# Kernel optimization log

Hardware: AMD Instinct MI355X
Metric: run time of the kernel (lower is better)

## Reference

```python
import jax, jax.numpy as jnp
import numpy as np

B, T, N, CIN, H, K, HOR = 64, 12, 800, 2, 64, 3, 12
TCOV_IN, TCOV_H, MNUM, MDIM = 60, 2, 4, 8
KAPPA = 0.05
IN0 = CIN + TCOV_H  # layer-0 input dim: data channels + time-covariate embedding


def setup_inputs() -> dict:
    key = jax.random.key(0)
    ks = jax.random.split(key, 24)
    def nrm(k, shape, s=0.1):
        return jax.random.normal(k, shape, jnp.float32) * s
    inp = {}
    inp["x_seq"] = jax.random.normal(ks[0], (B, T, N, CIN), jnp.float32)
    inp["t_x"] = jax.random.normal(ks[1], (B, T, TCOV_IN), jnp.float32)
    inp["t_y"] = jax.random.normal(ks[2], (B, HOR, TCOV_IN), jnp.float32)
    # adaptive graph as in init_adp_graph: softmax(relu(v1 @ v2), axis=1)
    inp["G"] = jax.nn.softmax(jax.nn.relu(nrm(ks[3], (N, 20), 1.0) @ nrm(ks[4], (20, N), 1.0)), axis=1)
    i = 5
    for pre in ("enc", "dec"):
        for l, hin in enumerate((IN0, H)):
            inp[f"{pre}_Wg{l}"] = nrm(ks[i], ((hin + H) * K, 2 * H)); i += 1
            inp[f"{pre}_bg{l}"] = jnp.zeros((2 * H,), jnp.float32)
            inp[f"{pre}_Wc{l}"] = nrm(ks[i], ((hin + H) * K, H)); i += 1
            inp[f"{pre}_bc{l}"] = jnp.zeros((H,), jnp.float32)
    inp["mlp_W1"] = nrm(ks[i], (TCOV_IN, 10)); i += 1
    inp["mlp_b1"] = jnp.zeros((10,), jnp.float32)
    inp["mlp_W2"] = nrm(ks[i], (10, TCOV_H * N)); i += 1
    inp["mlp_b2"] = jnp.zeros((TCOV_H * N,), jnp.float32)
    inp["memory"] = nrm(ks[i], (MNUM, MDIM), 1.0); i += 1
    inp["Wa"] = nrm(ks[i], (N * H, MDIM), 0.01); i += 1
    inp["fc"] = nrm(ks[i], (MDIM, MDIM * N), 0.1); i += 1
    inp["proj_W"] = nrm(ks[i], (H + MDIM, CIN)); i += 1
    inp["proj_b"] = jnp.zeros((CIN,), jnp.float32)
    return inp


def _cheby(G):
    # Chebyshev basis T_0..T_{K-1}: T_0=I, T_1=G, T_k = 2 G T_{k-1} - T_{k-2}
    Gs = [jnp.eye(N, dtype=G.dtype), G]
    for _ in range(2, K):
        Gs.append(2.0 * (G @ Gs[-1]) - Gs[-2])
    return jnp.stack(Gs[:K])  # (K, N, N)


def _gconv(x, Gs, W, b):
    # mixhop: h_k = kappa*x + (1-kappa) * einsum('bnp,nm->bmp', x, T_k); concat over k, then project
    agg = KAPPA * x[None] + (1.0 - KAPPA) * jnp.einsum('bnp,knm->kbmp', x, Gs)  # (K,B,N,P)
    Bq, Nq, P = x.shape
    h = jnp.transpose(agg, (1, 2, 0, 3)).reshape(Bq, Nq, K * P)  # matches torch.cat order
    return h @ W + b


def _cell(x, h, Gs, Wg, bg, Wc, bc):
    # GCRU cell: graph-conv GRU
    ur = _gconv(jnp.concatenate([x, h], -1), Gs, Wg, bg)
    u, r = jnp.split(ur, 2, axis=-1)
    u = jax.nn.sigmoid(u)
    r = jax.nn.sigmoid(r)
    c = jnp.tanh(_gconv(jnp.concatenate([x, r * h], -1), Gs, Wc, bc))
    return (1.0 - u) * h + u * c


def _mlp(t, W1, b1, W2, b2):
    # nn.Sequential(Linear, Linear) -- no activation in between
    return (t @ W1 + b1) @ W2 + b2


def reference(x_seq, t_x, t_y, G, enc_Wg0, enc_bg0, enc_Wc0, enc_bc0, enc_Wg1, enc_bg1, enc_Wc1, enc_bc1, dec_Wg0, dec_bg0, dec_Wc0, dec_bc0, dec_Wg1, dec_bg1, dec_Wc1, dec_bc1, mlp_W1, mlp_b1, mlp_W2, mlp_b2, memory, Wa, fc, proj_W, proj_b):
    Gs = _cheby(G)
    # time covariates for encoder input
    tx_emb = _mlp(t_x, mlp_W1, mlp_b1, mlp_W2, mlp_b2).reshape(B, T, N, TCOV_H)
    x = jnp.concatenate([x_seq, tx_emb], -1)  # (B,T,N,IN0)
    # encoder: scan over time per layer
    seq = jnp.swapaxes(x, 0, 1)  # (T,B,N,.)
    enc_params = [(enc_Wg0, enc_bg0, enc_Wc0, enc_bc0), (enc_Wg1, enc_bg1, enc_Wc1, enc_bc1)]
    h_last = []
    for (Wg, bg, Wc, bc) in enc_params:
        def step(h, xt, Wg=Wg, bg=bg, Wc=Wc, bc=bc):
            hn = _cell(xt, h, Gs, Wg, bg, Wc, bc)
            return hn, hn
        h0 = jnp.zeros((B, N, H), x.dtype)
        hT, seq = jax.lax.scan(step, h0, seq)
        h_last.append(hT)
    dec_params = [(dec_Wg0, dec_bg0, dec_Wc0, dec_bc0), (dec_Wg1, dec_bg1, dec_Wc1, dec_bc1)]
    ty = jnp.swapaxes(t_y, 0, 1)  # (HOR,B,TCOV_IN)

    def dec_step(carry, tyt):
        go, h0, h1 = carry
        tye = _mlp(tyt, mlp_W1, mlp_b1, mlp_W2, mlp_b2).reshape(B, N, TCOV_H)
        xin = jnp.concatenate([go, tye], -1)
        h0 = _cell(xin, h0, Gs, *dec_params[0])
        h1 = _cell(h0, h1, Gs, *dec_params[1])
        # query_st_memory
        q = h1.reshape(B, N * H) @ Wa  # (B, MDIM)
        att = jax.nn.softmax(q @ memory.T, axis=1)  # (B, MNUM)
        attm = ((att @ memory) @ fc).reshape(B, N, MDIM)
        out = jax.nn.relu(jnp.concatenate([h1, attm], -1) @ proj_W + proj_b)  # (B,N,CIN)
        return (out, h0, h1), out

    go0 = jnp.zeros((B, N, CIN), x.dtype)
    _, outs = jax.lax.scan(dec_step, (go0, h_last[0], h_last[1]), ty)
    return jnp.swapaxes(outs, 0, 1)  # (B,HOR,N,CIN)
```

## Files before the change

### kernel.cpp

```cpp
#include <hip/hip_runtime.h>
#include <math.h>

typedef _Float16 f16_t;
typedef _Float16 half8 __attribute__((ext_vector_type(8)));
typedef float f32x4 __attribute__((ext_vector_type(4)));


struct Params {
  const float *x_seq, *t_x, *t_y, *G;
  const float *Wraw[8], *bia[8];
  const float *mW1, *mb1, *mW2, *mb2, *mem, *Wa, *fc, *projW, *projb;
  float* dout;
  float *h0, *h1, *txe, *tye, *hidb, *partial, *Wat;
  f16_t *T2h, *Bpk, *Y0g, *Ybg, *Y0c, *Ybc, *Uh;
  f16_t* wsp[8];
};

__device__ __forceinline__ float sigm(float x) { return 1.0f / (1.0f + expf(-x)); }

__device__ __forceinline__ int xcd_swz(int orig, int nwg) {
  int q = nwg >> 3, r = nwg & 7, xcd = orig & 7, j = orig >> 3;
  return (xcd < r ? xcd * (q + 1) : r * (q + 1) + (xcd - r) * q) + j;
}

__device__ __forceinline__ void gload16(const void* g, void* l) {
  __builtin_amdgcn_global_load_lds((const __attribute__((address_space(1))) void*)g,
                                   (__attribute__((address_space(3))) void*)l, 16, 0, 0);
}


__global__ void __launch_bounds__(256) k_pre0(Params p) {
  int nt = gridDim.x * blockDim.x, id = blockIdx.x * blockDim.x + threadIdx.x;
  float4 z = {0.f, 0.f, 0.f, 0.f};
  for (int i = id; i < 64 * 64 * 200; i += nt) { ((float4*)p.h0)[i] = z; ((float4*)p.h1)[i] = z; }
  for (int w = 0; w < 8; ++w) {
    int layer = (w >> 1) & 1, cand = w & 1;
    int P = layer ? 128 : 68, NC = cand ? 64 : 128;
    const float* W = p.Wraw[w];
    f16_t* dst = p.wsp[w];
    int tot = 3 * NC * 128;
    for (int idx = id; idx < tot; idx += nt) {
      int s = idx / (NC * 128), rem = idx - s * (NC * 128);
      int c = rem >> 7, pp = rem & 127;
      float v = 0.f;
      if (pp < P) {
        if (s == 0)
          v = W[(size_t)pp * NC + c] + 0.05f * (W[(size_t)(P + pp) * NC + c] + W[(size_t)(2 * P + pp) * NC + c]);
        else
          v = 0.95f * W[(size_t)(s * P + pp) * NC + c];
      }
      dst[idx] = (f16_t)v;
    }
  }
  for (int idx = id; idx < 15360; idx += nt) {
    int half = idx / 7680, rem = idx - half * 7680;
    int r = rem / 10, j = rem - r * 10;
    const float* tin = half ? p.t_y : p.t_x;
    float a = p.mb1[j];
    for (int k = 0; k < 60; ++k) a += tin[(size_t)r * 60 + k] * p.mW1[k * 10 + j];
    p.hidb[idx] = a;
  }
  for (int idx = id; idx < 409600; idx += nt) {
    int c = idx / 6400, r2 = idx - c * 6400;
    int n = r2 >> 3, d = r2 & 7;
    p.Wat[idx] = p.Wa[((size_t)n * 64 + c) * 8 + d];
  }
}

__global__ void __launch_bounds__(256) k_pre1(Params p) {
  __shared__ float As[16 * 68];
  __shared__ float Bs[16 * 68];
  int tid = threadIdx.x, tx = tid & 15, ty = tid >> 4;
  const float* A = p.G;
  for (int tile = blockIdx.x; tile < 169; tile += gridDim.x) {
    int bx = tile % 13, by = tile / 13;
    int rowBase = by * 64, colBase = bx * 64;
    float acc[4][4] = {};
    for (int k0 = 0; k0 < 800; k0 += 16) {
      __syncthreads();
      for (int e = tid; e < 1024; e += 256) {
        int r = e >> 4, c = e & 15;
        int gr = rowBase + r;
        As[c * 68 + r] = (gr < 800) ? A[gr * 800 + k0 + c] : 0.f;
      }
      for (int e = tid; e < 1024; e += 256) {
        int r = e >> 6, c = e & 63;
        int gc = colBase + c;
        Bs[r * 68 + c] = (gc < 800) ? A[(k0 + r) * 800 + gc] : 0.f;
      }
      __syncthreads();
#pragma unroll
      for (int kk = 0; kk < 16; ++kk) {
        float4 a4 = *(const float4*)&As[kk * 68 + ty * 4];
        float4 b4 = *(const float4*)&Bs[kk * 68 + tx * 4];
        float av[4] = {a4.x, a4.y, a4.z, a4.w};
        float bv[4] = {b4.x, b4.y, b4.z, b4.w};
#pragma unroll
        for (int i = 0; i < 4; ++i)
#pragma unroll
          for (int j = 0; j < 4; ++j) acc[i][j] += av[i] * bv[j];
      }
    }
#pragma unroll
    for (int i = 0; i < 4; ++i) {
      int m = rowBase + ty * 4 + i;
      if (m >= 800) continue;
#pragma unroll
      for (int j = 0; j < 4; ++j) {
        int n = colBase + tx * 4 + j;
        if (n < 800) p.T2h[(size_t)m * 800 + n] = (f16_t)(2.f * acc[i][j] - (m == n ? 1.f : 0.f));
      }
    }
  }
  int nt = gridDim.x * blockDim.x, id = blockIdx.x * blockDim.x + threadIdx.x;
  for (int idx = id; idx < 2 * 768 * 1600; idx += nt) {
    int half = idx / (768 * 1600), rem = idx - half * (768 * 1600);
    int r = rem / 1600, o = rem - r * 1600;
    const float* hid = p.hidb + half * 7680;
    float* emb = half ? p.tye : p.txe;
    float a = p.mb2[o];
#pragma unroll
    for (int k = 0; k < 10; ++k) a += hid[r * 10 + k] * p.mW2[k * 1600 + o];
    emb[rem] = a;
  }
}

__global__ void __launch_bounds__(256) k_pre2(Params p) {
  int nt = gridDim.x * blockDim.x, id = blockIdx.x * blockDim.x + threadIdx.x;
  for (int idx = id; idx < 7 * 50 * 4096; idx += nt) {
    int nT = idx / 204800, rem = idx - nT * 204800;
    int ks = rem >> 12, i = rem & 4095;
    int kg = i >> 10, col = (i >> 3) & 127, e = i & 7;
    int k = ks * 32 + kg * 8 + e;
    int n = nT * 128 + col;
    f16_t v = (f16_t)0.f;
    if (n < 800) v = (k < 800) ? (f16_t)p.G[(size_t)k * 800 + n] : p.T2h[(size_t)(k - 800) * 800 + n];
    p.Bpk[idx] = v;
  }
}

template <int LAYER>
__global__ void __launch_bounds__(256, 3) g_small(Params p, int widx, int dec, int t) {
  __shared__ f16_t XS[128 * 136];
  unsigned* XS32 = (unsigned*)XS;
  int tid = threadIdx.x, lane = tid & 63, wid = tid >> 6;
  int lrow = lane & 15, lgrp = lane >> 4;
  int wm = wid >> 1, wn = wid & 1;
  int swz = xcd_swz(blockIdx.x, gridDim.x);
  int b = swz / 7, nBase = (swz % 7) * 128;
  const f16_t* __restrict__ wb = p.wsp[widx];
  const float* emb = dec ? p.tye : p.txe;

  {
    int rp = tid >> 3, n0 = (tid & 7) * 16;
    int ng = nBase + n0;
    bool nval = ng < 800;
    for (int pass = 0; pass < 2; ++pass) {
      float v[2][16];
#pragma unroll
      for (int par = 0; par < 2; ++par) {
        int cp = pass * 64 + 2 * rp + par;
        float* vv = v[par];
        if (!nval) {
#pragma unroll
          for (int i = 0; i < 16; ++i) vv[i] = 0.f;
        } else if (LAYER == 1) {
          const float* src = (cp < 64) ? p.h0 + ((size_t)(b * 64 + cp)) * 800 + ng
                                       : p.h1 + ((size_t)(b * 64 + cp - 64)) * 800 + ng;
#pragma unroll
          for (int q = 0; q < 4; ++q) {
            float4 f = *(const float4*)(src + q * 4);
            vv[q * 4 + 0] = f.x; vv[q * 4 + 1] = f.y; vv[q * 4 + 2] = f.z; vv[q * 4 + 3] = f.w;
          }
        } else {
          if (cp >= 68) {
#pragma unroll
            for (int i = 0; i < 16; ++i) vv[i] = 0.f;
          } else if (cp >= 4) {
            const float* src = p.h0 + ((size_t)(b * 64 + cp - 4)) * 800 + ng;
#pragma unroll
            for (int q = 0; q < 4; ++q) {
              float4 f = *(const float4*)(src + q * 4);
              vv[q * 4 + 0] = f.x; vv[q * 4 + 1] = f.y; vv[q * 4 + 2] = f.z; vv[q * 4 + 3] = f.w;
            }
          } else if (cp >= 2) {
#pragma unroll
            for (int i = 0; i < 16; ++i)
              vv[i] = emb[(size_t)(b * 12 + t) * 1600 + (ng + i) * 2 + (cp - 2)];
          } else {
            if (dec) {
              if (t == 0) {
#pragma unroll
                for (int i = 0; i < 16; ++i) vv[i] = 0.f;
              } else {
#pragma unroll
                for (int i = 0; i < 16; ++i)
                  vv[i] = p.dout[((size_t)(b * 12 + t - 1) * 800 + ng + i) * 2 + cp];
              }
            } else {
#pragma unroll
              for (int i = 0; i < 16; ++i)
                vv[i] = p.x_seq[((size_t)(b * 12 + t) * 800 + ng + i) * 2 + cp];
            }
          }
        }
      }
#pragma unroll
      for (int i = 0; i < 16; ++i) {
        union { f16_t h[2]; unsigned u; } pk;
        pk.h[0] = (f16_t)v[0][i];
        pk.h[1] = (f16_t)v[1][i];
        XS32[(n0 + i) * 68 + pass * 32 + rp] = pk.u;
      }
    }
  }
  __syncthreads();

  for (int s = 0; s < 3; ++s) {
    f32x4 acc[4][4];
#pragma unroll
    for (int i = 0; i < 4; ++i)
#pragma unroll
      for (int j = 0; j < 4; ++j) acc[i][j] = (f32x4){0.f, 0.f, 0.f, 0.f};
#pragma unroll
    for (int ks = 0; ks < 4; ++ks) {
      half8 fa[4], fx[4];
#pragma unroll
      for (int mf = 0; mf < 4; ++mf)
        fa[mf] = *(const half8*)(wb + ((size_t)(s * 128 + wm * 64 + mf * 16 + lrow) << 7) + ks * 32 + lgrp * 8);
#pragma unroll
      for (int nt = 0; nt < 4; ++nt)
        fx[nt] = *(const half8*)(XS + (wn * 64 + nt * 16 + lrow) * 136 + ks * 32 + lgrp * 8);
#pragma unroll
      for (int mf = 0; mf < 4; ++mf)
#pragma unroll
        for (int nt = 0; nt < 4; ++nt)
          acc[mf][nt] = __builtin_amdgcn_mfma_f32_16x16x32_f16(fa[mf], fx[nt], acc[mf][nt], 0, 0, 0);
    }
#pragma unroll
    for (int mf = 0; mf < 4; ++mf)
#pragma unroll
      for (int nt = 0; nt < 4; ++nt) {
        int n = nBase + wn * 64 + nt * 16 + lrow;
        if (n >= 800) continue;
#pragma unroll
        for (int j = 0; j < 4; ++j) {
          int c = wm * 64 + mf * 16 + lgrp * 4 + j;
          size_t r = (size_t)(b * 128 + c);
          f16_t val = (f16_t)acc[mf][nt][j];
          if (s == 0) {
            p.Y0g[r * 800 + n] = val;
          } else {
            int kp = (s - 1) * 800 + n;
            p.Ybg[((size_t)(kp >> 3) * 8192 + r) * 8 + (kp & 7)] = val;
          }
        }
      }
  }
}

template <int LAYER>
__global__ void __launch_bounds__(256, 4) g_biggate(Params p, int w0, int dec, int t, float* hcur) {
  constexpr int Pin = LAYER ? 64 : 4;
  __shared__ __align__(16) f16_t SH[18432];
  f16_t* AS = SH;
  f16_t* BS = SH + 6144;
  int tid = threadIdx.x, lane = tid & 63, w = tid >> 6;
  int lrow = lane & 15, lgrp = lane >> 4;
  int wm = w >> 1, wn = w & 1;
  int swz = xcd_swz(blockIdx.x, gridDim.x);
  int rt = swz / 7;
  int rBase = rt * 64;
  int nTile = swz % 7;
  int b = rt >> 1;
  int rhblk = rt & 1;
  const f16_t* __restrict__ Abase = p.Ybg;
  const f16_t* __restrict__ Bbase = p.Bpk + (size_t)nTile * 204800;
  const float* bias = p.bia[w0];

  auto stage = [&](int buf, int ks) {
    gload16(Abase + ((size_t)(ks * 4 + w) * 8192 + rBase + lane) * 8, AS + buf * 2048 + w * 512);
    gload16(Bbase + (size_t)ks * 4096 + (size_t)(w * 2 + 0) * 512 + lane * 8, BS + buf * 4096 + (w * 2 + 0) * 512);
    gload16(Bbase + (size_t)ks * 4096 + (size_t)(w * 2 + 1) * 512 + lane * 8, BS + buf * 4096 + (w * 2 + 1) * 512);
  };

  f32x4 acc[2][4];
#pragma unroll
  for (int i = 0; i < 2; ++i)
#pragma unroll
    for (int j = 0; j < 4; ++j) acc[i][j] = (f32x4){0.f, 0.f, 0.f, 0.f};

  stage(0, 0);
  stage(1, 1);
  for (int ks = 0; ks < 50; ++ks) {
    if (ks == 49) {
      asm volatile("s_waitcnt vmcnt(0)" ::: "memory");
    } else {
      asm volatile("s_waitcnt vmcnt(3)" ::: "memory");
    }
    __builtin_amdgcn_s_barrier();
    __builtin_amdgcn_sched_barrier(0);
    int cur = ks % 3;
    half8 fa[2], fb[4];
#pragma unroll
    for (int mt = 0; mt < 2; ++mt)
      fa[mt] = *(const half8*)(AS + cur * 2048 + lgrp * 512 + (wm * 32 + mt * 16 + lrow) * 8);
#pragma unroll
    for (int nt = 0; nt < 4; ++nt)
      fb[nt] = *(const half8*)(BS + cur * 4096 + lgrp * 1024 + (wn * 64 + nt * 16 + lrow) * 8);
    if (ks + 2 < 50) stage((ks + 2) % 3, ks + 2);
#pragma unroll
    for (int mt = 0; mt < 2; ++mt)
#pragma unroll
      for (int nt = 0; nt < 4; ++nt)
        acc[mt][nt] = __builtin_amdgcn_mfma_f32_16x16x32_f16(fa[mt], fb[nt], acc[mt][nt], 0, 0, 0);
  }

  if (!rhblk) {
#pragma unroll
    for (int mt = 0; mt < 2; ++mt)
#pragma unroll
      for (int nt = 0; nt < 4; ++nt) {
        int n = nTile * 128 + wn * 64 + nt * 16 + lrow;
        if (n >= 800) continue;
#pragma unroll
        for (int j = 0; j < 4; ++j) {
          int c = wm * 32 + mt * 16 + lgrp * 4 + j;
          int r = rBase + c;
          float v = acc[mt][nt][j] + (float)p.Y0g[(size_t)r * 800 + n] + bias[c];
          p.Uh[(size_t)(b * 64 + c) * 800 + n] = (f16_t)sigm(v);
        }
      }
    return;
  }

  f16_t rhv[2][4][4];
#pragma unroll
  for (int mt = 0; mt < 2; ++mt)
#pragma unroll
    for (int nt = 0; nt < 4; ++nt) {
      int n = nTile * 128 + wn * 64 + nt * 16 + lrow;
#pragma unroll
      for (int j = 0; j < 4; ++j) {
        int jj = wm * 32 + mt * 16 + lgrp * 4 + j;
        if (n < 800) {
          int r = rBase + jj;
          float v = acc[mt][nt][j] + (float)p.Y0g[(size_t)r * 800 + n] + bias[64 + jj];
          float hv = hcur[(size_t)(b * 64 + jj) * 800 + n];
          rhv[mt][nt][j] = (f16_t)(sigm(v) * hv);
        } else {
          rhv[mt][nt][j] = (f16_t)0.f;
        }
      }
    }

  __syncthreads();
  f16_t* Xc = SH;

#pragma unroll
  for (int mt = 0; mt < 2; ++mt)
#pragma unroll
    for (int nt = 0; nt < 4; ++nt) {
      int col = wn * 64 + nt * 16 + lrow;
#pragma unroll
      for (int j = 0; j < 4; ++j) {
        int jj = wm * 32 + mt * 16 + lgrp * 4 + j;
        Xc[col * 136 + Pin + jj] = rhv[mt][nt][j];
      }
    }
  if (LAYER == 1) {
    int ct = tid >> 2, nq = tid & 3;
    const float* src = p.h0 + (size_t)(b * 64 + ct) * 800;
#pragma unroll 8
    for (int i = 0; i < 32; ++i) {
      int nl = nq * 32 + i;
      int n = nTile * 128 + nl;
      float v = (n < 800) ? src[n] : 0.f;
      Xc[nl * 136 + ct] = (f16_t)v;
    }
  } else {
    if (tid < 128) {
      int col = tid;
      int n = nTile * 128 + col;
      float v0 = 0.f, v1 = 0.f, v2 = 0.f, v3 = 0.f;
      if (n < 800) {
        if (dec) {
          if (t > 0) {
            v0 = p.dout[((size_t)(b * 12 + t - 1) * 800 + n) * 2 + 0];
            v1 = p.dout[((size_t)(b * 12 + t - 1) * 800 + n) * 2 + 1];
          }
        } else {
          v0 = p.x_seq[((size_t)(b * 12 + t) * 800 + n) * 2 + 0];
          v1 = p.x_seq[((size_t)(b * 12 + t) * 800 + n) * 2 + 1];
        }
        const float* emb = dec ? p.tye : p.txe;
        v2 = emb[(size_t)(b * 12 + t) * 1600 + n * 2 + 0];
        v3 = emb[(size_t)(b * 12 + t) * 1600 + n * 2 + 1];
      }
      Xc[col * 136 + 0] = (f16_t)v0;
      Xc[col * 136 + 1] = (f16_t)v1;
      Xc[col * 136 + 2] = (f16_t)v2;
      Xc[col * 136 + 3] = (f16_t)v3;
      unsigned* z32 = (unsigned*)(Xc + col * 136 + 68);
#pragma unroll
      for (int q = 0; q < 30; ++q) z32[q] = 0u;
    }
  }
  __syncthreads();

  const f16_t* __restrict__ wc = p.wsp[w0 + 1];
  int cwn = w;
  for (int s = 0; s < 3; ++s) {
    f32x4 ac[4][2];
#pragma unroll
    for (int i = 0; i < 4; ++i)
#pragma unroll
      for (int j = 0; j < 2; ++j) ac[i][j] = (f32x4){0.f, 0.f, 0.f, 0.f};
#pragma unroll
    for (int ks = 0; ks < 4; ++ks) {
      half8 fa[4], fx[2];
#pragma unroll
      for (int mf = 0; mf < 4; ++mf)
        fa[mf] = *(const half8*)(wc + ((size_t)(s * 64 + mf * 16 + lrow) << 7) + ks * 32 + lgrp * 8);
#pragma unroll
      for (int nt = 0; nt < 2; ++nt)
        fx[nt] = *(const half8*)(Xc + (cwn * 32 + nt * 16 + lrow) * 136 + ks * 32 + lgrp * 8);
#pragma unroll
      for (int mf = 0; mf < 4; ++mf)
#pragma unroll
        for (int nt = 0; nt < 2; ++nt)
          ac[mf][nt] = __builtin_amdgcn_mfma_f32_16x16x32_f16(fa[mf], fx[nt], ac[mf][nt], 0, 0, 0);
    }
#pragma unroll
    for (int mf = 0; mf < 4; ++mf)
#pragma unroll
      for (int nt = 0; nt < 2; ++nt) {
        int n = nTile * 128 + cwn * 32 + nt * 16 + lrow;
        if (n >= 800) continue;
#pragma unroll
        for (int j = 0; j < 4; ++j) {
          int c = mf * 16 + lgrp * 4 + j;
          size_t r = (size_t)(b * 64 + c);
          f16_t val = (f16_t)ac[mf][nt][j];
          if (s == 0) {
            p.Y0c[r * 800 + n] = val;
          } else {
            int kp = (s - 1) * 800 + n;
            p.Ybc[((size_t)(kp >> 3) * 4096 + r) * 8 + (kp & 7)] = val;
          }
        }
      }
  }
}

__global__ void __launch_bounds__(256, 4) g_bigcand(Params p, int widx, float* hcur) {
  __shared__ __align__(16) f16_t SH[18432];
  f16_t* AS = SH;
  f16_t* BS = SH + 6144;
  int tid = threadIdx.x, lane = tid & 63, w = tid >> 6;
  int lrow = lane & 15, lgrp = lane >> 4;
  int wm = w >> 1, wn = w & 1;
  int swz = xcd_swz(blockIdx.x, gridDim.x);
  int rBase = (swz / 7) * 64;
  int nTile = swz % 7;
  const f16_t* __restrict__ Abase = p.Ybc;
  const f16_t* __restrict__ Bbase = p.Bpk + (size_t)nTile * 204800;
  const float* bias = p.bia[widx];

  auto stage = [&](int buf, int ks) {
    gload16(Abase + ((size_t)(ks * 4 + w) * 4096 + rBase + lane) * 8, AS + buf * 2048 + w * 512);
    gload16(Bbase + (size_t)ks * 4096 + (size_t)(w * 2 + 0) * 512 + lane * 8, BS + buf * 4096 + (w * 2 + 0) * 512);
    gload16(Bbase + (size_t)ks * 4096 + (size_t)(w * 2 + 1) * 512 + lane * 8, BS + buf * 4096 + (w * 2 + 1) * 512);
  };

  f32x4 acc[2][4];
#pragma unroll
  for (int i = 0; i < 2; ++i)
#pragma unroll
    for (int j = 0; j < 4; ++j) acc[i][j] = (f32x4){0.f, 0.f, 0.f, 0.f};

  stage(0, 0);
  stage(1, 1);
  for (int ks = 0; ks < 50; ++ks) {
    if (ks == 49) {
      asm volatile("s_waitcnt vmcnt(0)" ::: "memory");
    } else {
      asm volatile("s_waitcnt vmcnt(3)" ::: "memory");
    }
    __builtin_amdgcn_s_barrier();
    __builtin_amdgcn_sched_barrier(0);
    int cur = ks % 3;
    half8 fa[2], fb[4];
#pragma unroll
    for (int mt = 0; mt < 2; ++mt)
      fa[mt] = *(const half8*)(AS + cur * 2048 + lgrp * 512 + (wm * 32 + mt * 16 + lrow) * 8);
#pragma unroll
    for (int nt = 0; nt < 4; ++nt)
      fb[nt] = *(const half8*)(BS + cur * 4096 + lgrp * 1024 + (wn * 64 + nt * 16 + lrow) * 8);
    if (ks + 2 < 50) stage((ks + 2) % 3, ks + 2);
#pragma unroll
    for (int mt = 0; mt < 2; ++mt)
#pragma unroll
      for (int nt = 0; nt < 4; ++nt)
        acc[mt][nt] = __builtin_amdgcn_mfma_f32_16x16x32_f16(fa[mt], fb[nt], acc[mt][nt], 0, 0, 0);
  }

#pragma unroll
  for (int mt = 0; mt < 2; ++mt)
#pragma unroll
    for (int nt = 0; nt < 4; ++nt) {
      int n = nTile * 128 + wn * 64 + nt * 16 + lrow;
      if (n >= 800) continue;
#pragma unroll
      for (int j = 0; j < 4; ++j) {
        int r = rBase + wm * 32 + mt * 16 + lgrp * 4 + j;
        int b = r >> 6, c = r & 63;
        float v = acc[mt][nt][j] + (float)p.Y0c[(size_t)r * 800 + n] + bias[c];
        float u = (float)p.Uh[(size_t)(b * 64 + c) * 800 + n];
        float hv = hcur[(size_t)(b * 64 + c) * 800 + n];
        hcur[(size_t)(b * 64 + c) * 800 + n] = (1.f - u) * hv + u * tanhf(v);
      }
    }
}


__global__ void __launch_bounds__(256) k_att1(Params p) {
  int gwid = (blockIdx.x * blockDim.x + threadIdx.x) >> 6;
  int nw = (gridDim.x * blockDim.x) >> 6;
  int lane = threadIdx.x & 63;
  for (int tile = gwid; tile < 1024; tile += nw) {
    int cx = tile & 15, b = tile >> 4;
    float acc[8] = {};
    const float* hrow = p.h1 + (size_t)b * 51200 + cx * 3200;
    const float* wbase = p.Wat + (size_t)cx * 3200 * 8;
    for (int i = lane; i < 3200; i += 64) {
      float hv = hrow[i];
      const float* wr = wbase + (size_t)i * 8;
#pragma unroll
      for (int j = 0; j < 8; ++j) acc[j] += hv * wr[j];
    }
#pragma unroll
    for (int s = 1; s < 64; s <<= 1) {
#pragma unroll
      for (int j = 0; j < 8; ++j) acc[j] += __shfl_xor(acc[j], s);
    }
    if (lane == 0) {
#pragma unroll
      for (int j = 0; j < 8; ++j) p.partial[((size_t)b * 16 + cx) * 8 + j] = acc[j];
    }
  }
}

__global__ void __launch_bounds__(256) k_att2(Params p, int t) {
  int b = blockIdx.x >> 2, q4 = blockIdx.x & 3;
  int tid = threadIdx.x;
  float qv[8] = {};
  for (int cx = 0; cx < 16; ++cx)
#pragma unroll
    for (int j = 0; j < 8; ++j) qv[j] += p.partial[((size_t)b * 16 + cx) * 8 + j];
  float sco[4], mx = -1e30f;
#pragma unroll
  for (int m = 0; m < 4; ++m) {
    float s = 0.f;
#pragma unroll
    for (int d = 0; d < 8; ++d) s += qv[d] * p.mem[m * 8 + d];
    sco[m] = s;
    mx = fmaxf(mx, s);
  }
  float se = 0.f;
#pragma unroll
  for (int m = 0; m < 4; ++m) { sco[m] = expf(sco[m] - mx); se += sco[m]; }
  float attv[8];
#pragma unroll
  for (int d = 0; d < 8; ++d) {
    float av = 0.f;
#pragma unroll
    for (int m = 0; m < 4; ++m) av += (sco[m] / se) * p.mem[m * 8 + d];
    attv[d] = av;
  }
  if (tid >= 200) return;
  int n = q4 * 200 + tid;
  float attm[8];
#pragma unroll
  for (int d = 0; d < 8; ++d) {
    float s = 0.f;
#pragma unroll
    for (int m = 0; m < 8; ++m) s += attv[m] * p.fc[(size_t)m * 6400 + n * 8 + d];
    attm[d] = s;
  }
  float o0 = p.projb[0], o1 = p.projb[1];
  const float* hb = p.h1 + (size_t)b * 51200 + n;
#pragma unroll 16
  for (int j = 0; j < 64; ++j) {
    float hv = hb[(size_t)j * 800];
    o0 += hv * p.projW[j * 2 + 0];
    o1 += hv * p.projW[j * 2 + 1];
  }
#pragma unroll
  for (int d = 0; d < 8; ++d) {
    o0 += attm[d] * p.projW[(64 + d) * 2 + 0];
    o1 += attm[d] * p.projW[(64 + d) * 2 + 1];
  }
  size_t base = ((size_t)(b * 12 + t) * 800 + n) * 2;
  p.dout[base + 0] = fmaxf(o0, 0.f);
  p.dout[base + 1] = fmaxf(o1, 0.f);
}


extern "C" void kernel_launch(void* const* d_in, const int* in_sizes, int n_in,
                              void* d_out, int out_size, void* d_ws, size_t ws_size,
                              hipStream_t stream) {
  Params P;
  P.x_seq = (const float*)d_in[0];
  P.t_x = (const float*)d_in[1];
  P.t_y = (const float*)d_in[2];
  P.G = (const float*)d_in[3];
  P.Wraw[0] = (const float*)d_in[4];  P.bia[0] = (const float*)d_in[5];
  P.Wraw[1] = (const float*)d_in[6];  P.bia[1] = (const float*)d_in[7];
  P.Wraw[2] = (const float*)d_in[8];  P.bia[2] = (const float*)d_in[9];
  P.Wraw[3] = (const float*)d_in[10]; P.bia[3] = (const float*)d_in[11];
  P.Wraw[4] = (const float*)d_in[12]; P.bia[4] = (const float*)d_in[13];
  P.Wraw[5] = (const float*)d_in[14]; P.bia[5] = (const float*)d_in[15];
  P.Wraw[6] = (const float*)d_in[16]; P.bia[6] = (const float*)d_in[17];
  P.Wraw[7] = (const float*)d_in[18]; P.bia[7] = (const float*)d_in[19];
  P.mW1 = (const float*)d_in[20];
  P.mb1 = (const float*)d_in[21];
  P.mW2 = (const float*)d_in[22];
  P.mb2 = (const float*)d_in[23];
  P.mem = (const float*)d_in[24];
  P.Wa = (const float*)d_in[25];
  P.fc = (const float*)d_in[26];
  P.projW = (const float*)d_in[27];
  P.projb = (const float*)d_in[28];
  P.dout = (float*)d_out;

  float* ws = (float*)d_ws;
  size_t off = 0;
  auto alloc = [&](size_t nel) { float* q = ws + off; off += (nel + 3) & ~(size_t)3; return q; };
  P.T2h = (f16_t*)alloc(320000);
  P.Bpk = (f16_t*)alloc((size_t)7 * 50 * 4096 / 2);
  P.Y0g = (f16_t*)alloc((size_t)8192 * 800 / 2);
  P.Ybg = (f16_t*)alloc((size_t)1600 * 8192 / 2);
  P.Y0c = (f16_t*)alloc((size_t)4096 * 800 / 2);
  P.Ybc = (f16_t*)alloc((size_t)1600 * 4096 / 2);
  P.Uh = (f16_t*)alloc((size_t)4096 * 800 / 2);
  P.h0 = alloc((size_t)4096 * 800);
  P.h1 = alloc((size_t)4096 * 800);
  P.txe = alloc((size_t)768 * 1600);
  P.tye = alloc((size_t)768 * 1600);
  P.hidb = alloc(15360);
  P.partial = alloc(8192);
  P.Wat = alloc(409600);
  for (int w = 0; w < 8; ++w) {
    int cand = w & 1;
    int NC = cand ? 64 : 128;
    P.wsp[w] = (f16_t*)alloc((size_t)3 * NC * 128 / 2);
  }

  k_pre0<<<512, 256, 0, stream>>>(P);
  k_pre1<<<512, 256, 0, stream>>>(P);
  k_pre2<<<512, 256, 0, stream>>>(P);

  auto cell = [&](int dec, int t) {
    int w0 = dec * 4;
    g_small<0><<<448, 256, 0, stream>>>(P, w0 + 0, dec, t);
    g_biggate<0><<<896, 256, 0, stream>>>(P, w0 + 0, dec, t, P.h0);
    g_bigcand<<<448, 256, 0, stream>>>(P, w0 + 1, P.h0);
    g_small<1><<<448, 256, 0, stream>>>(P, w0 + 2, dec, t);
    g_biggate<1><<<896, 256, 0, stream>>>(P, w0 + 2, dec, t, P.h1);
    g_bigcand<<<448, 256, 0, stream>>>(P, w0 + 3, P.h1);
  };

  for (int t = 0; t < 12; ++t) cell(0, t);
  for (int t = 0; t < 12; ++t) {
    cell(1, t);
    k_att1<<<256, 256, 0, stream>>>(P);
    k_att2<<<256, 256, 0, stream>>>(P, t);
  }
}
```

Measured before the change: 6.594 ms.

## Fuse layer-1 small gconv into layer-0 candidate kernel and attention query into layer-1

The layer-0 candidate kernel now keeps the updated h0 tile in registers, stages it into shared memory together with h1, and runs the layer-1 gate-input small GEMM there. This removes the separate g_small<1> launch and its reread of h0. The layer-1 candidate kernel also computes the Wa attention-query partial sums in its epilogue and reduces them per block, which replaces k_att1. The cost is heavier epilogues, more per-thread Wat loads, and possible register pressure that lowers occupancy.

Result: slower. 7.338 ms (+11.3%).

```diff
diff --git a/kernel.cpp b/kernel.cpp
--- a/kernel.cpp
+++ b/kernel.cpp
@@ -139,8 +139,7 @@
   }
 }
 
-template <int LAYER>
-__global__ void __launch_bounds__(256, 3) g_small(Params p, int widx, int dec, int t) {
+__global__ void __launch_bounds__(256, 3) g_small0(Params p, int widx, int dec, int t) {
   __shared__ f16_t XS[128 * 136];
   unsigned* XS32 = (unsigned*)XS;
   int tid = threadIdx.x, lane = tid & 63, wid = tid >> 6;
@@ -161,47 +160,34 @@
       for (int par = 0; par < 2; ++par) {
         int cp = pass * 64 + 2 * rp + par;
         float* vv = v[par];
-        if (!nval) {
+        if (!nval || cp >= 68) {
 #pragma unroll
           for (int i = 0; i < 16; ++i) vv[i] = 0.f;
-        } else if (LAYER == 1) {
-          const float* src = (cp < 64) ? p.h0 + ((size_t)(b * 64 + cp)) * 800 + ng
-                                       : p.h1 + ((size_t)(b * 64 + cp - 64)) * 800 + ng;
+        } else if (cp >= 4) {
+          const float* src = p.h0 + ((size_t)(b * 64 + cp - 4)) * 800 + ng;
 #pragma unroll
           for (int q = 0; q < 4; ++q) {
             float4 f = *(const float4*)(src + q * 4);
             vv[q * 4 + 0] = f.x; vv[q * 4 + 1] = f.y; vv[q * 4 + 2] = f.z; vv[q * 4 + 3] = f.w;
           }
+        } else if (cp >= 2) {
+#pragma unroll
+          for (int i = 0; i < 16; ++i)
+            vv[i] = emb[(size_t)(b * 12 + t) * 1600 + (ng + i) * 2 + (cp - 2)];
         } else {
-          if (cp >= 68) {
-#pragma unroll
-            for (int i = 0; i < 16; ++i) vv[i] = 0.f;
-          } else if (cp >= 4) {
-            const float* src = p.h0 + ((size_t)(b * 64 + cp - 4)) * 800 + ng;
-#pragma unroll
-            for (int q = 0; q < 4; ++q) {
-              float4 f = *(const float4*)(src + q * 4);
-              vv[q * 4 + 0] = f.x; vv[q * 4 + 1] = f.y; vv[q * 4 + 2] = f.z; vv[q * 4 + 3] = f.w;
+          if (dec) {
+            if (t == 0) {
+#pragma unroll
+              for (int i = 0; i < 16; ++i) vv[i] = 0.f;
+            } else {
+#pragma unroll
+              for (int i = 0; i < 16; ++i)
+                vv[i] = p.dout[((size_t)(b * 12 + t - 1) * 800 + ng + i) * 2 + cp];
             }
-          } else if (cp >= 2) {
+          } else {
 #pragma unroll
             for (int i = 0; i < 16; ++i)
-              vv[i] = emb[(size_t)(b * 12 + t) * 1600 + (ng + i) * 2 + (cp - 2)];
-          } else {
-            if (dec) {
-              if (t == 0) {
-#pragma unroll
-                for (int i = 0; i < 16; ++i) vv[i] = 0.f;
-              } else {
-#pragma unroll
-                for (int i = 0; i < 16; ++i)
-                  vv[i] = p.dout[((size_t)(b * 12 + t - 1) * 800 + ng + i) * 2 + cp];
-              }
-            } else {
-#pragma unroll
-              for (int i = 0; i < 16; ++i)
-                vv[i] = p.x_seq[((size_t)(b * 12 + t) * 800 + ng + i) * 2 + cp];
-            }
+              vv[i] = p.x_seq[((size_t)(b * 12 + t) * 800 + ng + i) * 2 + cp];
           }
         }
       }
@@ -453,7 +439,7 @@
   }
 }
 
-__global__ void __launch_bounds__(256, 4) g_bigcand(Params p, int widx, float* hcur) {
+__global__ void __launch_bounds__(256, 4) g_bigcand0(Params p, int w0) {
   __shared__ __align__(16) f16_t SH[18432];
   f16_t* AS = SH;
   f16_t* BS = SH + 6144;
@@ -461,11 +447,12 @@
   int lrow = lane & 15, lgrp = lane >> 4;
   int wm = w >> 1, wn = w & 1;
   int swz = xcd_swz(blockIdx.x, gridDim.x);
-  int rBase = (swz / 7) * 64;
+  int b = swz / 7;
+  int rBase = b * 64;
   int nTile = swz % 7;
   const f16_t* __restrict__ Abase = p.Ybc;
   const f16_t* __restrict__ Bbase = p.Bpk + (size_t)nTile * 204800;
-  const float* bias = p.bia[widx];
+  const float* bias = p.bia[w0 + 1];
 
   auto stage = [&](int buf, int ks) {
     gload16(Abase + ((size_t)(ks * 4 + w) * 4096 + rBase + lane) * 8, AS + buf * 2048 + w * 512);
@@ -505,59 +492,206 @@
         acc[mt][nt] = __builtin_amdgcn_mfma_f32_16x16x32_f16(fa[mt], fb[nt], acc[mt][nt], 0, 0, 0);
   }
 
+  f16_t hnew[2][4][4];
 #pragma unroll
   for (int mt = 0; mt < 2; ++mt)
 #pragma unroll
     for (int nt = 0; nt < 4; ++nt) {
       int n = nTile * 128 + wn * 64 + nt * 16 + lrow;
-      if (n >= 800) continue;
 #pragma unroll
       for (int j = 0; j < 4; ++j) {
-        int r = rBase + wm * 32 + mt * 16 + lgrp * 4 + j;
-        int b = r >> 6, c = r & 63;
-        float v = acc[mt][nt][j] + (float)p.Y0c[(size_t)r * 800 + n] + bias[c];
-        float u = (float)p.Uh[(size_t)(b * 64 + c) * 800 + n];
-        float hv = hcur[(size_t)(b * 64 + c) * 800 + n];
-        hcur[(size_t)(b * 64 + c) * 800 + n] = (1.f - u) * hv + u * tanhf(v);
-      }
-    }
-}
-
-
-__global__ void __launch_bounds__(256) k_att1(Params p) {
-  int gwid = (blockIdx.x * blockDim.x + threadIdx.x) >> 6;
-  int nw = (gridDim.x * blockDim.x) >> 6;
-  int lane = threadIdx.x & 63;
-  for (int tile = gwid; tile < 1024; tile += nw) {
-    int cx = tile & 15, b = tile >> 4;
-    float acc[8] = {};
-    const float* hrow = p.h1 + (size_t)b * 51200 + cx * 3200;
-    const float* wbase = p.Wat + (size_t)cx * 3200 * 8;
-    for (int i = lane; i < 3200; i += 64) {
-      float hv = hrow[i];
-      const float* wr = wbase + (size_t)i * 8;
-#pragma unroll
-      for (int j = 0; j < 8; ++j) acc[j] += hv * wr[j];
-    }
+        int c = wm * 32 + mt * 16 + lgrp * 4 + j;
+        int r = rBase + c;
+        if (n < 800) {
+          float v = acc[mt][nt][j] + (float)p.Y0c[(size_t)r * 800 + n] + bias[c];
+          float u = (float)p.Uh[(size_t)(b * 64 + c) * 800 + n];
+          float hv = p.h0[(size_t)(b * 64 + c) * 800 + n];
+          float hn = (1.f - u) * hv + u * tanhf(v);
+          p.h0[(size_t)(b * 64 + c) * 800 + n] = hn;
+          hnew[mt][nt][j] = (f16_t)hn;
+        } else {
+          hnew[mt][nt][j] = (f16_t)0.f;
+        }
+      }
+    }
+
+  __syncthreads();
+  f16_t* Xs = SH;
+
+#pragma unroll
+  for (int mt = 0; mt < 2; ++mt)
+#pragma unroll
+    for (int nt = 0; nt < 4; ++nt) {
+      int col = wn * 64 + nt * 16 + lrow;
+#pragma unroll
+      for (int j = 0; j < 4; ++j) {
+        int c = wm * 32 + mt * 16 + lgrp * 4 + j;
+        Xs[col * 136 + c] = hnew[mt][nt][j];
+      }
+    }
+  {
+    int ct = tid >> 2, nq = tid & 3;
+    const float* src = p.h1 + (size_t)(b * 64 + ct) * 800;
+#pragma unroll 8
+    for (int i = 0; i < 32; ++i) {
+      int nl = nq * 32 + i;
+      int n = nTile * 128 + nl;
+      float v = (n < 800) ? src[n] : 0.f;
+      Xs[nl * 136 + 64 + ct] = (f16_t)v;
+    }
+  }
+  __syncthreads();
+
+  const f16_t* __restrict__ wb = p.wsp[w0 + 2];
+  for (int s = 0; s < 3; ++s) {
+    f32x4 ac[4][4];
+#pragma unroll
+    for (int i = 0; i < 4; ++i)
+#pragma unroll
+      for (int j = 0; j < 4; ++j) ac[i][j] = (f32x4){0.f, 0.f, 0.f, 0.f};
+#pragma unroll
+    for (int ks = 0; ks < 4; ++ks) {
+      half8 fa[4], fx[4];
+#pragma unroll
+      for (int mf = 0; mf < 4; ++mf)
+        fa[mf] = *(const half8*)(wb + ((size_t)(s * 128 + wm * 64 + mf * 16 + lrow) << 7) + ks * 32 + lgrp * 8);
+#pragma unroll
+      for (int nt = 0; nt < 4; ++nt)
+        fx[nt] = *(const half8*)(Xs + (wn * 64 + nt * 16 + lrow) * 136 + ks * 32 + lgrp * 8);
+#pragma unroll
+      for (int mf = 0; mf < 4; ++mf)
+#pragma unroll
+        for (int nt = 0; nt < 4; ++nt)
+          ac[mf][nt] = __builtin_amdgcn_mfma_f32_16x16x32_f16(fa[mf], fx[nt], ac[mf][nt], 0, 0, 0);
+    }
+#pragma unroll
+    for (int mf = 0; mf < 4; ++mf)
+#pragma unroll
+      for (int nt = 0; nt < 4; ++nt) {
+        int n = nTile * 128 + wn * 64 + nt * 16 + lrow;
+        if (n >= 800) continue;
+#pragma unroll
+        for (int j = 0; j < 4; ++j) {
+          int c = wm * 64 + mf * 16 + lgrp * 4 + j;
+          size_t r = (size_t)(b * 128 + c);
+          f16_t val = (f16_t)ac[mf][nt][j];
+          if (s == 0) {
+            p.Y0g[r * 800 + n] = val;
+          } else {
+            int kp = (s - 1) * 800 + n;
+            p.Ybg[((size_t)(kp >> 3) * 8192 + r) * 8 + (kp & 7)] = val;
+          }
+        }
+      }
+  }
+}
+
+__global__ void __launch_bounds__(256, 4) g_bigcand1(Params p, int w0, int doatt) {
+  __shared__ __align__(16) f16_t SH[18432];
+  f16_t* AS = SH;
+  f16_t* BS = SH + 6144;
+  int tid = threadIdx.x, lane = tid & 63, w = tid >> 6;
+  int lrow = lane & 15, lgrp = lane >> 4;
+  int wm = w >> 1, wn = w & 1;
+  int swz = xcd_swz(blockIdx.x, gridDim.x);
+  int b = swz / 7;
+  int rBase = b * 64;
+  int nTile = swz % 7;
+  const f16_t* __restrict__ Abase = p.Ybc;
+  const f16_t* __restrict__ Bbase = p.Bpk + (size_t)nTile * 204800;
+  const float* bias = p.bia[w0 + 3];
+
+  auto stage = [&](int buf, int ks) {
+    gload16(Abase + ((size_t)(ks * 4 + w) * 4096 + rBase + lane) * 8, AS + buf * 2048 + w * 512);
+    gload16(Bbase + (size_t)ks * 4096 + (size_t)(w * 2 + 0) * 512 + lane * 8, BS + buf * 4096 + (w * 2 + 0) * 512);
+    gload16(Bbase + (size_t)ks * 4096 + (size_t)(w * 2 + 1) * 512 + lane * 8, BS + buf * 4096 + (w * 2 + 1) * 512);
+  };
+
+  f32x4 acc[2][4];
+#pragma unroll
+  for (int i = 0; i < 2; ++i)
+#pragma unroll
+    for (int j = 0; j < 4; ++j) acc[i][j] = (f32x4){0.f, 0.f, 0.f, 0.f};
+
+  stage(0, 0);
+  stage(1, 1);
+  for (int ks = 0; ks < 50; ++ks) {
+    if (ks == 49) {
+      asm volatile("s_waitcnt vmcnt(0)" ::: "memory");
+    } else {
+      asm volatile("s_waitcnt vmcnt(3)" ::: "memory");
+    }
+    __builtin_amdgcn_s_barrier();
+    __builtin_amdgcn_sched_barrier(0);
+    int cur = ks % 3;
+    half8 fa[2], fb[4];
+#pragma unroll
+    for (int mt = 0; mt < 2; ++mt)
+      fa[mt] = *(const half8*)(AS + cur * 2048 + lgrp * 512 + (wm * 32 + mt * 16 + lrow) * 8);
+#pragma unroll
+    for (int nt = 0; nt < 4; ++nt)
+      fb[nt] = *(const half8*)(BS + cur * 4096 + lgrp * 1024 + (wn * 64 + nt * 16 + lrow) * 8);
+    if (ks + 2 < 50) stage((ks + 2) % 3, ks + 2);
+#pragma unroll
+    for (int mt = 0; mt < 2; ++mt)
+#pragma unroll
+      for (int nt = 0; nt < 4; ++nt)
+        acc[mt][nt] = __builtin_amdgcn_mfma_f32_16x16x32_f16(fa[mt], fb[nt], acc[mt][nt], 0, 0, 0);
+  }
+
+  float qd[8] = {};
+#pragma unroll
+  for (int mt = 0; mt < 2; ++mt)
+#pragma unroll
+    for (int nt = 0; nt < 4; ++nt) {
+      int n = nTile * 128 + wn * 64 + nt * 16 + lrow;
+#pragma unroll
+      for (int j = 0; j < 4; ++j) {
+        int c = wm * 32 + mt * 16 + lgrp * 4 + j;
+        if (n < 800) {
+          float v = acc[mt][nt][j] + (float)p.Y0c[(size_t)(rBase + c) * 800 + n] + bias[c];
+          float u = (float)p.Uh[(size_t)(b * 64 + c) * 800 + n];
+          float hv = p.h1[(size_t)(b * 64 + c) * 800 + n];
+          float hn = (1.f - u) * hv + u * tanhf(v);
+          p.h1[(size_t)(b * 64 + c) * 800 + n] = hn;
+          if (doatt) {
+            const float* wr = p.Wat + ((size_t)c * 800 + n) * 8;
+#pragma unroll
+            for (int d = 0; d < 8; ++d) qd[d] += hn * wr[d];
+          }
+        }
+      }
+    }
+
+  if (doatt) {
 #pragma unroll
     for (int s = 1; s < 64; s <<= 1) {
 #pragma unroll
-      for (int j = 0; j < 8; ++j) acc[j] += __shfl_xor(acc[j], s);
-    }
+      for (int d = 0; d < 8; ++d) qd[d] += __shfl_xor(qd[d], s);
+    }
+    __syncthreads();
+    float* red = (float*)SH;
     if (lane == 0) {
 #pragma unroll
-      for (int j = 0; j < 8; ++j) p.partial[((size_t)b * 16 + cx) * 8 + j] = acc[j];
-    }
-  }
-}
+      for (int d = 0; d < 8; ++d) red[w * 8 + d] = qd[d];
+    }
+    __syncthreads();
+    if (tid == 0) {
+#pragma unroll
+      for (int d = 0; d < 8; ++d)
+        p.partial[((size_t)b * 7 + nTile) * 8 + d] = red[d] + red[8 + d] + red[16 + d] + red[24 + d];
+    }
+  }
+}
+
 
 __global__ void __launch_bounds__(256) k_att2(Params p, int t) {
   int b = blockIdx.x >> 2, q4 = blockIdx.x & 3;
   int tid = threadIdx.x;
   float qv[8] = {};
-  for (int cx = 0; cx < 16; ++cx)
-#pragma unroll
-    for (int j = 0; j < 8; ++j) qv[j] += p.partial[((size_t)b * 16 + cx) * 8 + j];
+  for (int cx = 0; cx < 7; ++cx)
+#pragma unroll
+    for (int j = 0; j < 8; ++j) qv[j] += p.partial[((size_t)b * 7 + cx) * 8 + j];
   float sco[4], mx = -1e30f;
 #pragma unroll
   for (int m = 0; m < 4; ++m) {
@@ -649,7 +783,7 @@
   P.txe = alloc((size_t)768 * 1600);
   P.tye = alloc((size_t)768 * 1600);
   P.hidb = alloc(15360);
-  P.partial = alloc(8192);
+  P.partial = alloc(64 * 7 * 8);
   P.Wat = alloc(409600);
   for (int w = 0; w < 8; ++w) {
     int cand = w & 1;
@@ -663,18 +797,16 @@
 
   auto cell = [&](int dec, int t) {
     int w0 = dec * 4;
-    g_small<0><<<448, 256, 0, stream>>>(P, w0 + 0, dec, t);
+    g_small0<<<448, 256, 0, stream>>>(P, w0 + 0, dec, t);
     g_biggate<0><<<896, 256, 0, stream>>>(P, w0 + 0, dec, t, P.h0);
-    g_bigcand<<<448, 256, 0, stream>>>(P, w0 + 1, P.h0);
-    g_small<1><<<448, 256, 0, stream>>>(P, w0 + 2, dec, t);
+    g_bigcand0<<<448, 256, 0, stream>>>(P, w0);
     g_biggate<1><<<896, 256, 0, stream>>>(P, w0 + 2, dec, t, P.h1);
-    g_bigcand<<<448, 256, 0, stream>>>(P, w0 + 3, P.h1);
+    g_bigcand1<<<448, 256, 0, stream>>>(P, w0, dec);
   };
 
   for (int t = 0; t < 12; ++t) cell(0, t);
   for (int t = 0; t < 12; ++t) {
     cell(1, t);
-    k_att1<<<256, 256, 0, stream>>>(P);
     k_att2<<<256, 256, 0, stream>>>(P, t);
   }
 }
```
